# Kernel optimization log

Hardware: AMD Instinct MI355X
Metric: run time of the kernel (lower is better)

Reference implementation:

```python
import math
import jax, jax.numpy as jnp
import numpy as np

B, T, DIN, DH, E, TOPK = 2048, 512, 32, 96, 6, 2


def setup_inputs() -> dict:
    key = jax.random.key(0)
    ks = jax.random.split(key, 20)
    x = jax.random.normal(ks[0], (B, T, DIN), jnp.float32)
    lengths = jax.random.randint(ks[1], (B,), 1, T + 1)
    mask = (jnp.arange(T)[None, :] < lengths[:, None])

    def U(k, shape, fan):
        s = 1.0 / math.sqrt(fan)
        return jax.random.uniform(k, shape, jnp.float32, -s, s)

    # PyTorch LSTM init: U(-1/sqrt(DH), 1/sqrt(DH)); gate order i,f,g,o
    Wih = U(ks[2], (4 * DH, DIN), DH)
    Whh = U(ks[3], (4 * DH, DH), DH)
    bih = U(ks[4], (4 * DH,), DH)
    bhh = U(ks[5], (4 * DH,), DH)
    Wq = U(ks[6], (DH, DH), DH); bq = U(ks[7], (DH,), DH)
    Wk = U(ks[8], (DH, DH), DH); bk = U(ks[9], (DH,), DH)
    Wv = U(ks[10], (DH, DH), DH); bv = U(ks[11], (DH,), DH)
    Wg = U(ks[12], (E, 2 * DH), 2 * DH); bg = U(ks[13], (E,), 2 * DH)
    We1 = U(ks[14], (E, DH, 2 * DH), 2 * DH); be1 = U(ks[15], (E, DH), 2 * DH)
    We2 = U(ks[16], (E, DH), DH); be2 = U(ks[17], (E,), DH)
    return dict(x=x, lengths=lengths, mask=mask, Wih=Wih, Whh=Whh, bih=bih, bhh=bhh,
                Wq=Wq, bq=bq, Wk=Wk, bk=bk, Wv=Wv, bv=bv, Wg=Wg, bg=bg,
                We1=We1, be1=be1, We2=We2, be2=be2)


def _lstm(x, mask, Wih, Whh, bih, bhh):
    # packed-sequence semantics: carry frozen past each sample's length,
    # padded output positions zeroed (like pad_packed_sequence).
    xg = x @ Wih.T + bih  # [B,T,4*DH] precomputed input projection
    dh = Whh.shape[1]

    def step(carry, inp):
        h, c = carry
        xg_t, m_t = inp
        g = xg_t + h @ Whh.T + bhh
        i, f, gg, o = jnp.split(g, 4, axis=-1)
        c_new = jax.nn.sigmoid(f) * c + jax.nn.sigmoid(i) * jnp.tanh(gg)
        h_new = jax.nn.sigmoid(o) * jnp.tanh(c_new)
        m = m_t[:, None]
        h = jnp.where(m, h_new, h)
        c = jnp.where(m, c_new, c)
        return (h, c), jnp.where(m, h_new, 0.0)

    init = (jnp.zeros((x.shape[0], dh), x.dtype), jnp.zeros((x.shape[0], dh), x.dtype))
    (hT, _), H = jax.lax.scan(step, init, (jnp.swapaxes(xg, 0, 1), mask.T))
    return jnp.swapaxes(H, 0, 1), hT  # H:[B,T,DH], hT:[B,DH]


def reference(x, lengths, mask, Wih, Whh, bih, bhh, Wq, bq, Wk, bk, Wv, bv,
              Wg, bg, We1, be1, We2, be2):
    H, hT = _lstm(x, mask, Wih, Whh, bih, bhh)
    Q = hT @ Wq.T + bq                      # [B,DH]
    K = H @ Wk.T + bk                       # [B,T,DH]
    V = H @ Wv.T + bv                       # [B,T,DH]
    logits = jnp.einsum('bd,btd->bt', Q, K) / math.sqrt(K.shape[-1])
    logits = jnp.where(mask, logits, -1e9)
    alpha = jax.nn.softmax(logits, axis=1)  # [B,T]
    ctx = jnp.einsum('bt,btd->bd', alpha, V)
    feats = jnp.concatenate([ctx, hT], axis=-1)  # [B,2*DH]
    gate_logits = feats @ Wg.T + bg              # [B,E]
    topv, topi = jax.lax.top_k(gate_logits, TOPK)
    pi = jax.nn.softmax(topv, axis=-1)           # [B,TOPK]
    # all-expert dense compute (E tiny), then gather selected -> same math as
    # the per-expert masked scatter loop in the torch module (dropout off).
    h1 = jax.nn.relu(jnp.einsum('bf,ehf->beh', feats, We1) + be1[None])  # [B,E,DH]
    outs = jnp.einsum('beh,eh->be', h1, We2) + be2[None]                  # [B,E]
    sel = jnp.take_along_axis(outs, topi, axis=1)                         # [B,TOPK]
    yhat = jnp.sum(pi * sel, axis=-1, keepdims=True)                      # [B,1]
    return yhat, alpha, gate_logits
```

## Files before the change

kernel.cpp:

```cpp
#include <hip/hip_runtime.h>
#include <hip/hip_bf16.h>

#define B_ 2048
#define T_ 512
#define DIN_ 32
#define DH_ 96
#define NG_ 384
#define E_ 6

#define BPB 8
#define HP 104
#define GS 8

typedef __attribute__((ext_vector_type(8))) _Float16 f16x8;
typedef __attribute__((ext_vector_type(4))) float f32x4;

#if defined(__has_builtin)
# if __has_builtin(__builtin_amdgcn_exp2f)
#  define EXP2F(x) __builtin_amdgcn_exp2f(x)
# endif
# if __has_builtin(__builtin_amdgcn_rcpf)
#  define RCPF(x) __builtin_amdgcn_rcpf(x)
# endif
#endif
#ifndef EXP2F
# define EXP2F(x) exp2f(x)
#endif
#ifndef RCPF
# define RCPF(x) (1.0f/(x))
#endif

__device__ __forceinline__ float sigf(float x) {
    return RCPF(1.0f + EXP2F(x * -1.44269504f));
}
__device__ __forceinline__ float tanhf_(float x) {
    return 1.0f - 2.0f * RCPF(1.0f + EXP2F(x * 2.88539008f));
}

__device__ __forceinline__ f16x8 cvt8(float4 a, float4 b) {
    f16x8 r;
    r[0] = (_Float16)a.x; r[1] = (_Float16)a.y; r[2] = (_Float16)a.z; r[3] = (_Float16)a.w;
    r[4] = (_Float16)b.x; r[5] = (_Float16)b.y; r[6] = (_Float16)b.z; r[7] = (_Float16)b.w;
    return r;
}
__device__ __forceinline__ f16x8 cvt8p(const float* p) {
    return cvt8(*(const float4*)p, *(const float4*)(p + 4));
}

__device__ __forceinline__ void lds_barrier() {
    asm volatile("s_waitcnt lgkmcnt(0)\n\ts_barrier" ::: "memory");
}

__global__ __launch_bounds__(512) void sort_zero_kernel(int* __restrict__ bins) {
    bins[threadIdx.x] = 0;
}
__global__ __launch_bounds__(256) void sort_count_kernel(
    const int* __restrict__ lengths, int* __restrict__ bins) {
    const int b = blockIdx.x * 256 + threadIdx.x;
    atomicAdd(&bins[lengths[b] - 1], 1);
}
__global__ __launch_bounds__(512) void sort_scan_kernel(
    const int* __restrict__ bins, int* __restrict__ offs) {
    __shared__ int s[512];
    const int tid = threadIdx.x;
    s[tid] = bins[tid];
    __syncthreads();
    for (int d = 1; d < 512; d <<= 1) {
        int v = (tid >= d) ? s[tid - d] : 0;
        __syncthreads();
        s[tid] += v;
        __syncthreads();
    }
    offs[tid] = s[tid] - bins[tid];
}
__global__ __launch_bounds__(256) void sort_place_kernel(
    const int* __restrict__ lengths, int* __restrict__ offs,
    int* __restrict__ perm) {
    const int b = blockIdx.x * 256 + threadIdx.x;
    const int pos = atomicAdd(&offs[lengths[b] - 1], 1);
    perm[pos] = b;
}

__global__ __launch_bounds__(768, 1) void lstm_kernel(
    const float* __restrict__ x, const int* __restrict__ lengths,
    const int* __restrict__ perm,
    const float* __restrict__ Wih, const float* __restrict__ Whh,
    const float* __restrict__ bih, const float* __restrict__ bhh,
    _Float16* __restrict__ Hout, float* __restrict__ hT)
{
    __shared__ float sgate[NG_ * GS];
    __shared__ _Float16 sh[2][16 * HP];
    __shared__ int sgb[BPB], slen[BPB];

    const int tid  = threadIdx.x;
    const int bb   = blockIdx.x * BPB;
    const int wave = tid >> 6;
    const int lane = tid & 63;
    const int col  = lane & 15;
    const int quad = lane >> 4;

    if (tid < BPB) {
        const int g = perm[bb + tid];
        sgb[tid] = g;
        slen[tid] = lengths[g];
    }
    {
        _Float16* shf = &sh[0][0];
        for (int i = tid; i < 2 * 16 * HP; i += 768) shf[i] = (_Float16)0.f;
    }
    __syncthreads();

    int bmax = slen[0];
#pragma unroll
    for (int i = 1; i < BPB; ++i) bmax = max(bmax, slen[i]);

    int gc[2]; float bias[2];
    f16x8 wh[2][3], wi[2];
#pragma unroll
    for (int j = 0; j < 2; ++j) {
        const int tau = wave * 2 + j;
        const int g = tau / 6, u6 = tau % 6;
        const int gcj = g * DH_ + u6 * 16 + col;
        gc[j] = gcj;
#pragma unroll
        for (int kf = 0; kf < 3; ++kf)
            wh[j][kf] = cvt8p(Whh + gcj * DH_ + kf * 32 + quad * 8);
        wi[j] = cvt8p(Wih + gcj * DIN_ + quad * 8);
        bias[j] = bih[gcj] + bhh[gcj];
    }

    const int eu = tid >> 3;
    const int eb = tid & 7;
    float c1 = 0.f, hk1 = 0.f;
    const int len1 = slen[eb];

    const bool st_act = tid < 384;
    const int sb = tid / 48;
    const int su = (tid % 48) * 2;
    _Float16* Hst = Hout + ((long long)sgb[sb] * T_) * DH_ + su;

    const float* xp = x + ((long long)sgb[col & 7] * T_) * DIN_ + quad * 8;
    float4 xc0 = *(const float4*)xp;
    float4 xc1 = *(const float4*)(xp + 4);

    for (int t = 0; t < bmax; ++t) {
        const int buf = t & 1;

        const _Float16* hrow = &sh[buf][col * HP];
        f16x8 h0 = *(const f16x8*)(hrow + 0  + quad * 8);
        f16x8 h1 = *(const f16x8*)(hrow + 32 + quad * 8);
        f16x8 h2 = *(const f16x8*)(hrow + 64 + quad * 8);

        const float* xpn = (t + 1 < T_) ? (xp + DIN_) : xp;
        float4 xn0 = *(const float4*)xpn;
        float4 xn1 = *(const float4*)(xpn + 4);

        f16x8 xa = cvt8(xc0, xc1);

#pragma unroll
        for (int j = 0; j < 2; ++j) {
            f32x4 a = {bias[j], bias[j], bias[j], bias[j]};
            a = __builtin_amdgcn_mfma_f32_16x16x32_f16(h0, wh[j][0], a, 0, 0, 0);
            a = __builtin_amdgcn_mfma_f32_16x16x32_f16(h1, wh[j][1], a, 0, 0, 0);
            a = __builtin_amdgcn_mfma_f32_16x16x32_f16(h2, wh[j][2], a, 0, 0, 0);
            a = __builtin_amdgcn_mfma_f32_16x16x32_f16(xa, wi[j],    a, 0, 0, 0);
            if (quad < 2)
                *(f32x4*)&sgate[gc[j] * GS + quad * 4] = a;
        }
        lds_barrier();

        if (t > 0 && st_act) {
            unsigned v = *(const unsigned*)&sh[buf][sb * HP + su];
            *(unsigned*)Hst = v;
            Hst += DH_;
        }

        {
            float iv = sgate[(0 * DH_ + eu) * GS + eb];
            float fv = sgate[(1 * DH_ + eu) * GS + eb];
            float gv = sgate[(2 * DH_ + eu) * GS + eb];
            float ov = sgate[(3 * DH_ + eu) * GS + eb];
            float cn = sigf(fv) * c1 + sigf(iv) * tanhf_(gv);
            float hn = sigf(ov) * tanhf_(cn);
            const bool m = t < len1;
            c1  = m ? cn : c1;
            hk1 = m ? hn : hk1;
            sh[buf ^ 1][eb * HP + eu] = (_Float16)hk1;
        }
        lds_barrier();

        xp = xpn; xc0 = xn0; xc1 = xn1;
    }

    if (st_act) {
        unsigned v = *(const unsigned*)&sh[bmax & 1][sb * HP + su];
        *(unsigned*)Hst = v;
    }

    hT[sgb[eb] * DH_ + eu] = hk1;
}

__global__ __launch_bounds__(128) void qk_kernel(
    const float* __restrict__ hT, const float* __restrict__ Wq,
    const float* __restrict__ bq, const float* __restrict__ Wk,
    const float* __restrict__ bk, float* __restrict__ qk_out,
    float* __restrict__ qb_out)
{
    __shared__ float shT[DH_], sQ[DH_];
    const int b = blockIdx.x, tid = threadIdx.x;
    const float scale = 0.10206207262f;
    if (tid < DH_) shT[tid] = hT[b * DH_ + tid];
    __syncthreads();
    if (tid < DH_) {
        float acc = bq[tid];
        const float* wr = Wq + tid * DH_;
        for (int d = 0; d < DH_; d += 4) {
            float4 w4 = *(const float4*)(wr + d);
            acc += w4.x * shT[d] + w4.y * shT[d + 1] + w4.z * shT[d + 2] + w4.w * shT[d + 3];
        }
        sQ[tid] = acc;
    }
    __syncthreads();
    if (tid < DH_) {
        float acc = 0.f;
        for (int j = 0; j < DH_; ++j) acc += Wk[j * DH_ + tid] * sQ[j];
        qk_out[b * DH_ + tid] = acc * scale;
    }
    if (tid == 0) {
        float acc = 0.f;
        for (int d = 0; d < DH_; ++d) acc += sQ[d] * bk[d];
        qb_out[b] = acc * scale;
    }
}

__global__ __launch_bounds__(512) void attn_moe_kernel(
    const _Float16* __restrict__ H, const float* __restrict__ hT,
    const float* __restrict__ qk, const float* __restrict__ qb,
    const int* __restrict__ lengths,
    const float* __restrict__ Wv, const float* __restrict__ bv,
    const float* __restrict__ Wg, const float* __restrict__ bg,
    const float* __restrict__ We1, const float* __restrict__ be1,
    const float* __restrict__ We2, const float* __restrict__ be2,
    float* __restrict__ yhat_out, float* __restrict__ alpha_out,
    float* __restrict__ gl_out)
{
    __shared__ float salpha[T_];
    __shared__ float sqk[DH_];
    __shared__ float spart[4 * DH_];
    __shared__ float sfeats[2 * DH_];
    __shared__ float sh1[2][DH_];
    __shared__ float sred[8], ssum[8];
    __shared__ float sgl[E_];
    __shared__ float spi[2];
    __shared__ int stopi[2];

    const int b = blockIdx.x, tid = threadIdx.x;
    const int len = lengths[b];
    if (tid < DH_) sqk[tid] = qk[b * DH_ + tid];
    const float qbv = qb[b];
    __syncthreads();

    const bool valid = tid < len;
    float l = qbv;
    if (valid) {
        const _Float16* hr = H + ((long long)b * T_ + tid) * DH_;
#pragma unroll
        for (int u = 0; u < DH_; u += 8) {
            f16x8 hv = *(const f16x8*)(hr + u);
            float4 qa = *(const float4*)&sqk[u];
            float4 qc = *(const float4*)&sqk[u + 4];
            l += (float)hv[0] * qa.x + (float)hv[1] * qa.y
               + (float)hv[2] * qa.z + (float)hv[3] * qa.w
               + (float)hv[4] * qc.x + (float)hv[5] * qc.y
               + (float)hv[6] * qc.z + (float)hv[7] * qc.w;
        }
    }
    float lv = valid ? l : -1e30f;

    float m = lv;
    for (int off = 32; off; off >>= 1) m = fmaxf(m, __shfl_xor(m, off));
    if ((tid & 63) == 0) sred[tid >> 6] = m;
    __syncthreads();
    m = sred[0];
#pragma unroll
    for (int i = 1; i < 8; ++i) m = fmaxf(m, sred[i]);

    float e = valid ? EXP2F((l - m) * 1.44269504f) : 0.f;
    float s = e;
    for (int off = 32; off; off >>= 1) s += __shfl_xor(s, off);
    if ((tid & 63) == 0) ssum[tid >> 6] = s;
    __syncthreads();
    s = ssum[0];
#pragma unroll
    for (int i = 1; i < 8; ++i) s += ssum[i];

    const float alpha = e * RCPF(s);
    salpha[tid] = alpha;
    alpha_out[(long long)b * T_ + tid] = alpha;
    __syncthreads();

    if (tid < 4 * DH_) {
        const int s4 = tid / DH_, u = tid - s4 * DH_;
        float acc = 0.f;
        const int t0 = s4 * 128, t1 = min(t0 + 128, len);
        const _Float16* hc = H + ((long long)b * T_) * DH_ + u;
        for (int t = t0; t < t1; ++t)
            acc += salpha[t] * (float)hc[t * DH_];
        spart[s4 * DH_ + u] = acc;
    }
    __syncthreads();
    if (tid < DH_) {
        float craw = spart[tid] + spart[DH_ + tid] + spart[2 * DH_ + tid] + spart[3 * DH_ + tid];
        spart[tid] = craw;
    }
    __syncthreads();
    if (tid < DH_) {
        float acc = bv[tid];
        const float* wr = Wv + tid * DH_;
        for (int u = 0; u < DH_; u += 4) {
            float4 w4 = *(const float4*)(wr + u);
            acc += w4.x * spart[u] + w4.y * spart[u + 1] + w4.z * spart[u + 2] + w4.w * spart[u + 3];
        }
        sfeats[tid] = acc;
        sfeats[DH_ + tid] = hT[b * DH_ + tid];
    }
    __syncthreads();

    if (tid < 192) {
        const int e6 = tid >> 5, cc = tid & 31;
        float p = 0.f;
        const float* wg = Wg + e6 * 2 * DH_;
#pragma unroll
        for (int j = 0; j < 6; ++j) p += wg[cc * 6 + j] * sfeats[cc * 6 + j];
        for (int off = 16; off; off >>= 1) p += __shfl_xor(p, off);
        if (cc == 0) {
            float g = p + bg[e6];
            sgl[e6] = g;
            gl_out[b * E_ + e6] = g;
        }
    }
    __syncthreads();

    if (tid == 0) {
        int i0 = 0; float v0 = sgl[0];
        for (int ee = 1; ee < E_; ++ee) if (sgl[ee] > v0) { v0 = sgl[ee]; i0 = ee; }
        int i1 = -1; float v1 = -1e30f;
        for (int ee = 0; ee < E_; ++ee) {
            if (ee == i0) continue;
            if (sgl[ee] > v1) { v1 = sgl[ee]; i1 = ee; }
        }
        float e1 = EXP2F((v1 - v0) * 1.44269504f);
        float inv = RCPF(1.f + e1);
        spi[0] = inv; spi[1] = e1 * inv;
        stopi[0] = i0; stopi[1] = i1;
    }
    __syncthreads();

    if (tid < 192) {
        const int e2 = tid / DH_, u = tid - e2 * DH_;
        const int ex = stopi[e2];
        float acc = be1[ex * DH_ + u];
        const float* w = We1 + ((long long)ex * DH_ + u) * (2 * DH_);
        for (int f = 0; f < 2 * DH_; f += 4) {
            float4 w4 = *(const float4*)(w + f);
            acc += w4.x * sfeats[f] + w4.y * sfeats[f + 1] + w4.z * sfeats[f + 2] + w4.w * sfeats[f + 3];
        }
        sh1[e2][u] = fmaxf(acc, 0.f);
    }
    __syncthreads();

    if (tid == 0) {
        float outs[2];
#pragma unroll
        for (int e2 = 0; e2 < 2; ++e2) {
            const int ex = stopi[e2];
            float a = be2[ex];
            for (int u = 0; u < DH_; ++u) a += sh1[e2][u] * We2[ex * DH_ + u];
            outs[e2] = a;
        }
        yhat_out[b] = spi[0] * outs[0] + spi[1] * outs[1];
    }
}

extern "C" void kernel_launch(void* const* d_in, const int* in_sizes, int n_in,
                              void* d_out, int out_size, void* d_ws, size_t ws_size,
                              hipStream_t stream) {
    const float* x   = (const float*)d_in[0];
    const int* lengths = (const int*)d_in[1];
    const float* Wih = (const float*)d_in[3];
    const float* Whh = (const float*)d_in[4];
    const float* bih = (const float*)d_in[5];
    const float* bhh = (const float*)d_in[6];
    const float* Wq  = (const float*)d_in[7];
    const float* bq  = (const float*)d_in[8];
    const float* Wk  = (const float*)d_in[9];
    const float* bk  = (const float*)d_in[10];
    const float* Wv  = (const float*)d_in[11];
    const float* bv  = (const float*)d_in[12];
    const float* Wg  = (const float*)d_in[13];
    const float* bg  = (const float*)d_in[14];
    const float* We1 = (const float*)d_in[15];
    const float* be1 = (const float*)d_in[16];
    const float* We2 = (const float*)d_in[17];
    const float* be2 = (const float*)d_in[18];

    float* yhat  = (float*)d_out;
    float* alpha = yhat + B_;
    float* gl    = alpha + (size_t)B_ * T_;

    char* ws = (char*)d_ws;
    _Float16* Hws = (_Float16*)ws;
    float* hTws = (float*)(ws + (size_t)B_ * T_ * DH_ * 2);
    float* qkws = hTws + (size_t)B_ * DH_;
    float* qbws = qkws + (size_t)B_ * DH_;
    int* bins   = (int*)(qbws + B_);
    int* offs   = bins + 512;
    int* perm   = offs + 512;

    sort_zero_kernel<<<dim3(1), dim3(512), 0, stream>>>(bins);
    sort_count_kernel<<<dim3(B_ / 256), dim3(256), 0, stream>>>(lengths, bins);
    sort_scan_kernel<<<dim3(1), dim3(512), 0, stream>>>(bins, offs);
    sort_place_kernel<<<dim3(B_ / 256), dim3(256), 0, stream>>>(lengths, offs, perm);

    lstm_kernel<<<dim3(B_ / BPB), dim3(768), 0, stream>>>(
        x, lengths, perm, Wih, Whh, bih, bhh, Hws, hTws);
    qk_kernel<<<dim3(B_), dim3(128), 0, stream>>>(
        hTws, Wq, bq, Wk, bk, qkws, qbws);
    attn_moe_kernel<<<dim3(B_), dim3(512), 0, stream>>>(
        Hws, hTws, qkws, qbws, lengths, Wv, bv, Wg, bg,
        We1, be1, We2, be2, yhat, alpha, gl);
}
```

Baseline: 805.8 us.

## Fuse sort and qk kernels, pad gate LDS stride, parallelize expert output

Merges the four counting-sort launches into one single-block kernel that works in shared memory, and folds the Q/K projection kernel into the attention/MoE kernel so Q·Wk and Q·bk are computed per block. Changes the LDS gate stride from 8 to 10 with float2 stores, presumably to reduce bank conflicts in the LSTM step. Replaces the single-thread expert output dot product with wave-level shuffle reductions. The aim is to cut launch overhead and serial work, at the cost of a serial single-block sort and redundant Wq/Wk reads per block.

```diff
diff --git a/kernel.cpp b/kernel.cpp
--- a/kernel.cpp
+++ b/kernel.cpp
@@ -10,7 +10,7 @@
 
 #define BPB 8
 #define HP 104
-#define GS 8
+#define GS 10
 
 typedef __attribute__((ext_vector_type(8))) _Float16 f16x8;
 typedef __attribute__((ext_vector_type(4))) float f32x4;
@@ -51,34 +51,31 @@
     asm volatile("s_waitcnt lgkmcnt(0)\n\ts_barrier" ::: "memory");
 }
 
-__global__ __launch_bounds__(512) void sort_zero_kernel(int* __restrict__ bins) {
-    bins[threadIdx.x] = 0;
-}
-__global__ __launch_bounds__(256) void sort_count_kernel(
-    const int* __restrict__ lengths, int* __restrict__ bins) {
-    const int b = blockIdx.x * 256 + threadIdx.x;
-    atomicAdd(&bins[lengths[b] - 1], 1);
-}
-__global__ __launch_bounds__(512) void sort_scan_kernel(
-    const int* __restrict__ bins, int* __restrict__ offs) {
-    __shared__ int s[512];
+__global__ __launch_bounds__(512) void sort_kernel(
+    const int* __restrict__ lengths, int* __restrict__ perm) {
+    __shared__ int sbins[512];
+    __shared__ int soffs[512];
     const int tid = threadIdx.x;
-    s[tid] = bins[tid];
+    sbins[tid] = 0;
+    __syncthreads();
+    for (int b = tid; b < B_; b += 512) atomicAdd(&sbins[lengths[b] - 1], 1);
+    __syncthreads();
+    soffs[tid] = sbins[tid];
     __syncthreads();
     for (int d = 1; d < 512; d <<= 1) {
-        int v = (tid >= d) ? s[tid - d] : 0;
+        int v = (tid >= d) ? soffs[tid - d] : 0;
         __syncthreads();
-        s[tid] += v;
+        soffs[tid] += v;
         __syncthreads();
     }
-    offs[tid] = s[tid] - bins[tid];
-}
-__global__ __launch_bounds__(256) void sort_place_kernel(
-    const int* __restrict__ lengths, int* __restrict__ offs,
-    int* __restrict__ perm) {
-    const int b = blockIdx.x * 256 + threadIdx.x;
-    const int pos = atomicAdd(&offs[lengths[b] - 1], 1);
-    perm[pos] = b;
+    int excl = soffs[tid] - sbins[tid];
+    __syncthreads();
+    soffs[tid] = excl;
+    __syncthreads();
+    for (int b = tid; b < B_; b += 512) {
+        const int pos = atomicAdd(&soffs[lengths[b] - 1], 1);
+        perm[pos] = b;
+    }
 }
 
 __global__ __launch_bounds__(768, 1) void lstm_kernel(
@@ -164,8 +161,11 @@
             a = __builtin_amdgcn_mfma_f32_16x16x32_f16(h1, wh[j][1], a, 0, 0, 0);
             a = __builtin_amdgcn_mfma_f32_16x16x32_f16(h2, wh[j][2], a, 0, 0, 0);
             a = __builtin_amdgcn_mfma_f32_16x16x32_f16(xa, wi[j],    a, 0, 0, 0);
-            if (quad < 2)
-                *(f32x4*)&sgate[gc[j] * GS + quad * 4] = a;
+            if (quad < 2) {
+                float2* sp = (float2*)&sgate[gc[j] * GS + quad * 4];
+                sp[0] = float2{a[0], a[1]};
+                sp[1] = float2{a[2], a[3]};
+            }
         }
         lds_barrier();
 
@@ -200,43 +200,11 @@
     hT[sgb[eb] * DH_ + eu] = hk1;
 }
 
-__global__ __launch_bounds__(128) void qk_kernel(
-    const float* __restrict__ hT, const float* __restrict__ Wq,
-    const float* __restrict__ bq, const float* __restrict__ Wk,
-    const float* __restrict__ bk, float* __restrict__ qk_out,
-    float* __restrict__ qb_out)
-{
-    __shared__ float shT[DH_], sQ[DH_];
-    const int b = blockIdx.x, tid = threadIdx.x;
-    const float scale = 0.10206207262f;
-    if (tid < DH_) shT[tid] = hT[b * DH_ + tid];
-    __syncthreads();
-    if (tid < DH_) {
-        float acc = bq[tid];
-        const float* wr = Wq + tid * DH_;
-        for (int d = 0; d < DH_; d += 4) {
-            float4 w4 = *(const float4*)(wr + d);
-            acc += w4.x * shT[d] + w4.y * shT[d + 1] + w4.z * shT[d + 2] + w4.w * shT[d + 3];
-        }
-        sQ[tid] = acc;
-    }
-    __syncthreads();
-    if (tid < DH_) {
-        float acc = 0.f;
-        for (int j = 0; j < DH_; ++j) acc += Wk[j * DH_ + tid] * sQ[j];
-        qk_out[b * DH_ + tid] = acc * scale;
-    }
-    if (tid == 0) {
-        float acc = 0.f;
-        for (int d = 0; d < DH_; ++d) acc += sQ[d] * bk[d];
-        qb_out[b] = acc * scale;
-    }
-}
-
 __global__ __launch_bounds__(512) void attn_moe_kernel(
     const _Float16* __restrict__ H, const float* __restrict__ hT,
-    const float* __restrict__ qk, const float* __restrict__ qb,
     const int* __restrict__ lengths,
+    const float* __restrict__ Wq, const float* __restrict__ bq,
+    const float* __restrict__ Wk, const float* __restrict__ bk,
     const float* __restrict__ Wv, const float* __restrict__ bv,
     const float* __restrict__ Wg, const float* __restrict__ bg,
     const float* __restrict__ We1, const float* __restrict__ be1,
@@ -245,6 +213,8 @@
     float* __restrict__ gl_out)
 {
     __shared__ float salpha[T_];
+    __shared__ float shT[DH_];
+    __shared__ float sQ[DH_];
     __shared__ float sqk[DH_];
     __shared__ float spart[4 * DH_];
     __shared__ float sfeats[2 * DH_];
@@ -252,13 +222,40 @@
     __shared__ float sred[8], ssum[8];
     __shared__ float sgl[E_];
     __shared__ float spi[2];
+    __shared__ float souts[2];
+    __shared__ float sqb_s;
     __shared__ int stopi[2];
 
     const int b = blockIdx.x, tid = threadIdx.x;
     const int len = lengths[b];
-    if (tid < DH_) sqk[tid] = qk[b * DH_ + tid];
-    const float qbv = qb[b];
-    __syncthreads();
+    const float scale = 0.10206207262f;
+
+    if (tid < DH_) shT[tid] = hT[b * DH_ + tid];
+    __syncthreads();
+    if (tid < DH_) {
+        float acc = bq[tid];
+        const float* wr = Wq + tid * DH_;
+        for (int d = 0; d < DH_; d += 4) {
+            float4 w4 = *(const float4*)(wr + d);
+            acc += w4.x * shT[d] + w4.y * shT[d + 1] + w4.z * shT[d + 2] + w4.w * shT[d + 3];
+        }
+        sQ[tid] = acc;
+    }
+    __syncthreads();
+    if (tid < DH_) {
+        float acc = 0.f;
+        for (int j = 0; j < DH_; ++j) acc += Wk[j * DH_ + tid] * sQ[j];
+        sqk[tid] = acc * scale;
+    }
+    if (tid >= 448) {
+        const int ln = tid - 448;
+        float p = sQ[ln] * bk[ln];
+        if (ln < DH_ - 64) p += sQ[ln + 64] * bk[ln + 64];
+        for (int off = 32; off; off >>= 1) p += __shfl_xor(p, off);
+        if (ln == 0) sqb_s = p * scale;
+    }
+    __syncthreads();
+    const float qbv = sqb_s;
 
     const bool valid = tid < len;
     float l = qbv;
@@ -322,7 +319,7 @@
             acc += w4.x * spart[u] + w4.y * spart[u + 1] + w4.z * spart[u + 2] + w4.w * spart[u + 3];
         }
         sfeats[tid] = acc;
-        sfeats[DH_ + tid] = hT[b * DH_ + tid];
+        sfeats[DH_ + tid] = shT[tid];
     }
     __syncthreads();
 
@@ -369,17 +366,18 @@
     }
     __syncthreads();
 
-    if (tid == 0) {
-        float outs[2];
-#pragma unroll
-        for (int e2 = 0; e2 < 2; ++e2) {
-            const int ex = stopi[e2];
-            float a = be2[ex];
-            for (int u = 0; u < DH_; ++u) a += sh1[e2][u] * We2[ex * DH_ + u];
-            outs[e2] = a;
-        }
-        yhat_out[b] = spi[0] * outs[0] + spi[1] * outs[1];
-    }
+    if (tid < 128) {
+        const int e2 = tid >> 6, ln = tid & 63;
+        const int ex = stopi[e2];
+        const float* w2 = We2 + ex * DH_;
+        float p = sh1[e2][ln] * w2[ln];
+        if (ln < DH_ - 64) p += sh1[e2][ln + 64] * w2[ln + 64];
+        for (int off = 32; off; off >>= 1) p += __shfl_xor(p, off);
+        if (ln == 0) souts[e2] = p + be2[ex];
+    }
+    __syncthreads();
+    if (tid == 0)
+        yhat_out[b] = spi[0] * souts[0] + spi[1] * souts[1];
 }
 
 extern "C" void kernel_launch(void* const* d_in, const int* in_sizes, int n_in,
@@ -417,16 +415,11 @@
     int* offs   = bins + 512;
     int* perm   = offs + 512;
 
-    sort_zero_kernel<<<dim3(1), dim3(512), 0, stream>>>(bins);
-    sort_count_kernel<<<dim3(B_ / 256), dim3(256), 0, stream>>>(lengths, bins);
-    sort_scan_kernel<<<dim3(1), dim3(512), 0, stream>>>(bins, offs);
-    sort_place_kernel<<<dim3(B_ / 256), dim3(256), 0, stream>>>(lengths, offs, perm);
+    sort_kernel<<<dim3(1), dim3(512), 0, stream>>>(lengths, perm);
 
     lstm_kernel<<<dim3(B_ / BPB), dim3(768), 0, stream>>>(
         x, lengths, perm, Wih, Whh, bih, bhh, Hws, hTws);
-    qk_kernel<<<dim3(B_), dim3(128), 0, stream>>>(
-        hTws, Wq, bq, Wk, bk, qkws, qbws);
     attn_moe_kernel<<<dim3(B_), dim3(512), 0, stream>>>(
-        Hws, hTws, qkws, qbws, lengths, Wv, bv, Wg, bg,
+        Hws, hTws, lengths, Wq, bq, Wk, bk, Wv, bv, Wg, bg,
         We1, be1, We2, be2, yhat, alpha, gl);
 }
```

After: 781.2 us. 1.03x faster.
